# Kernel tuning notes

Hardware: AMD Instinct MI355X
Metric: run time of the kernel (lower is better)

The kernel has to match this reference:

```python
import jax, jax.numpy as jnp
import numpy as np

KERNEL_PARA = 1.0

def setup_inputs() -> dict:
    key = jax.random.key(0)
    k1, k2 = jax.random.split(key)
    H1 = jax.random.normal(k1, (8192, 64), dtype=jnp.float32)
    H2 = jax.random.normal(k2, (8192, 64), dtype=jnp.float32)
    return {"H1": H1, "H2": H2}

def reference(H1, H2):
    # S[ij] = exp(-delta * ||x_i - x_j||^2), via ||a||^2 + ||b||^2 - 2 a.b
    H11 = jnp.sum(H1 * H1, axis=1)[:, None]          # [n1, 1]
    H22 = jnp.sum(H2 * H2, axis=1)[None, :]          # [1, n2]
    H12 = jnp.matmul(H1, H2.T)                        # [n1, n2]
    D_2 = H11 + H22 - 2.0 * H12
    return jnp.exp(-KERNEL_PARA * D_2)
```

## Files before the change

### kernel.cpp

```cpp
#include <hip/hip_runtime.h>
#include <hip/hip_bf16.h>


typedef float  f32x4   __attribute__((ext_vector_type(4)));
typedef float  float4v __attribute__((ext_vector_type(4)));
typedef short  short8  __attribute__((ext_vector_type(8)));
typedef unsigned short ushort8 __attribute__((ext_vector_type(8)));

#define TM 128
#define TN 128
#define KD 64

__device__ __forceinline__ unsigned short f2bf(float x) {
    __hip_bfloat16 h = __float2bfloat16(x);
    unsigned short u;
    __builtin_memcpy(&u, &h, 2);
    return u;
}
__device__ __forceinline__ float bf2f(unsigned short u) {
    unsigned int v = ((unsigned int)u) << 16;
    float f;
    __builtin_memcpy(&f, &v, 4);
    return f;
}

__global__ __launch_bounds__(256, 2) void gauss_mfma(
    const float* __restrict__ H1, const float* __restrict__ H2,
    float* __restrict__ out, int N1, int N2)
{
    __shared__ __align__(16) unsigned short sAhi[TM * KD];
    __shared__ __align__(16) unsigned short sAlo[TM * KD];
    __shared__ __align__(16) unsigned short sBhi[TN * KD];
    __shared__ __align__(16) unsigned short sBlo[TN * KD];
    __shared__ float snrm[TM + TN];

    const int t = threadIdx.x;
    const int row0 = blockIdx.y * TM;
    const int col0 = blockIdx.x * TN;

    #pragma unroll
    for (int side = 0; side < 2; ++side) {
        const float* src = side ? (H2 + (size_t)col0 * KD)
                                : (H1 + (size_t)row0 * KD);
        unsigned short* hi = side ? sBhi : sAhi;
        unsigned short* lo = side ? sBlo : sAlo;
        #pragma unroll
        for (int i = 0; i < 4; ++i) {
            int g   = i * 256 + t;
            int row = g >> 3;
            int kc  = g & 7;
            const float4v* p = (const float4v*)(src + (size_t)g * 8);
            float4v v0 = p[0], v1 = p[1];
            ushort8 h, l;
            #pragma unroll
            for (int e = 0; e < 8; ++e) {
                float a = (e < 4) ? v0[e] : v1[e - 4];
                unsigned short hb = f2bf(a);
                float r = a - bf2f(hb);
                h[e] = hb;
                l[e] = f2bf(r);
            }
            unsigned int off = (unsigned)(row * (KD * 2) + kc * 16);
            off ^= (unsigned)((row & 7) << 4);
            *(ushort8*)((char*)hi + off) = h;
            *(ushort8*)((char*)lo + off) = l;
        }
    }
    __syncthreads();

    {
        const unsigned short* hi = (t < TM) ? sAhi : sBhi;
        const unsigned short* lo = (t < TM) ? sAlo : sBlo;
        int row = (t < TM) ? t : (t - TM);
        float s = 0.f;
        #pragma unroll
        for (int kc = 0; kc < 8; ++kc) {
            unsigned int off = (unsigned)(row * (KD * 2) + kc * 16)
                             ^ (unsigned)((row & 7) << 4);
            ushort8 h = *(const ushort8*)((const char*)hi + off);
            ushort8 l = *(const ushort8*)((const char*)lo + off);
            #pragma unroll
            for (int e = 0; e < 8; ++e) {
                float a = bf2f(h[e]) + bf2f(l[e]);
                s = fmaf(a, a, s);
            }
        }
        snrm[t] = s;
    }
    __syncthreads();

    const int lane = t & 63;
    const int w    = t >> 6;
    const int wr   = w >> 1, wc = w & 1;
    const int lr   = lane & 15;
    const int kb   = lane >> 4;

    f32x4 acc[4][4];
    #pragma unroll
    for (int a = 0; a < 4; ++a)
        #pragma unroll
        for (int b = 0; b < 4; ++b)
            acc[a][b] = (f32x4){0.f, 0.f, 0.f, 0.f};

    #pragma unroll
    for (int ks = 0; ks < 2; ++ks) {
        short8 bh[4], bl[4];
        #pragma unroll
        for (int fc = 0; fc < 4; ++fc) {
            int rowb = wc * 64 + fc * 16 + lr;
            unsigned int off = (unsigned)(rowb * (KD * 2) + ks * 64 + kb * 16)
                             ^ (unsigned)((rowb & 7) << 4);
            bh[fc] = *(const short8*)((const char*)sBhi + off);
            bl[fc] = *(const short8*)((const char*)sBlo + off);
        }
        #pragma unroll
        for (int fr = 0; fr < 4; ++fr) {
            int rowa = wr * 64 + fr * 16 + lr;
            unsigned int off = (unsigned)(rowa * (KD * 2) + ks * 64 + kb * 16)
                             ^ (unsigned)((rowa & 7) << 4);
            short8 ah = *(const short8*)((const char*)sAhi + off);
            short8 al = *(const short8*)((const char*)sAlo + off);
            #pragma unroll
            for (int fc = 0; fc < 4; ++fc) {
                acc[fr][fc] = __builtin_amdgcn_mfma_f32_16x16x32_bf16(
                                  ah, bh[fc], acc[fr][fc], 0, 0, 0);
                acc[fr][fc] = __builtin_amdgcn_mfma_f32_16x16x32_bf16(
                                  ah, bl[fc], acc[fr][fc], 0, 0, 0);
                acc[fr][fc] = __builtin_amdgcn_mfma_f32_16x16x32_bf16(
                                  al, bh[fc], acc[fr][fc], 0, 0, 0);
            }
        }
    }

    const int r4 = (lane >> 4) * 4;
    #pragma unroll
    for (int fr = 0; fr < 4; ++fr) {
        int rloc = wr * 64 + fr * 16 + r4;
        #pragma unroll
        for (int fc = 0; fc < 4; ++fc) {
            int cloc = wc * 64 + fc * 16 + lr;
            float n2v = snrm[TM + cloc];
            size_t gc = (size_t)(col0 + cloc);
            #pragma unroll
            for (int j = 0; j < 4; ++j) {
                float n1v = snrm[rloc + j];
                float d2  = n1v + n2v - 2.0f * acc[fr][fc][j];
                out[(size_t)(row0 + rloc + j) * (size_t)N2 + gc] = __expf(-d2);
            }
        }
    }
}

extern "C" void kernel_launch(void* const* d_in, const int* in_sizes, int n_in,
                              void* d_out, int out_size, void* d_ws, size_t ws_size,
                              hipStream_t stream) {
    const float* H1 = (const float*)d_in[0];
    const float* H2 = (const float*)d_in[1];
    float* out = (float*)d_out;
    const int n1 = in_sizes[0] / KD;
    const int n2 = in_sizes[1] / KD;
    dim3 grid(n2 / TN, n1 / TM);
    gauss_mfma<<<grid, dim3(256), 0, stream>>>(H1, H2, out, n1, n2);
}
```

Measured before the change: 56.59 us.

## Precompute bf16 hi/lo planes and norms in prep kernel, stage via direct LDS loads

Adds a prep kernel that splits H1/H2 into bf16 hi/lo panels already in the swizzled LDS layout and computes the row norms once into the workspace. The main kernel then copies those panels straight into LDS with global_load_lds, so each of the 4096 tiles no longer repeats the conversion and norm work. It also swaps the MFMA operand order so every lane ends up holding 4 contiguous output columns, which allows vectorized nontemporal stores. The cost is an extra launch plus workspace traffic, and the old path remains as a fallback when the workspace is too small.

```diff
diff --git a/kernel.cpp b/kernel.cpp
--- a/kernel.cpp
+++ b/kernel.cpp
@@ -2,14 +2,18 @@
 #include <hip/hip_bf16.h>
 
 
-typedef float  f32x4   __attribute__((ext_vector_type(4)));
-typedef float  float4v __attribute__((ext_vector_type(4)));
-typedef short  short8  __attribute__((ext_vector_type(8)));
+typedef float  f32x4  __attribute__((ext_vector_type(4)));
+typedef short  short8 __attribute__((ext_vector_type(8)));
 typedef unsigned short ushort8 __attribute__((ext_vector_type(8)));
 
+#define KD 64
 #define TM 128
 #define TN 128
-#define KD 64
+
+#define PLANE_BYTES (8192u * 64u * 2u)
+#define OFF_N1  (4u * PLANE_BYTES)
+#define OFF_N2  (4u * PLANE_BYTES + 8192u * 4u)
+#define WS_NEED ((size_t)(4u * PLANE_BYTES + 2u * 8192u * 4u))
 
 __device__ __forceinline__ unsigned short f2bf(float x) {
     __hip_bfloat16 h = __float2bfloat16(x);
@@ -24,76 +28,142 @@
     return f;
 }
 
-__global__ __launch_bounds__(256, 2) void gauss_mfma(
-    const float* __restrict__ H1, const float* __restrict__ H2,
-    float* __restrict__ out, int N1, int N2)
+__device__ __forceinline__ void gload_lds16(const void* g, void* l) {
+    __builtin_amdgcn_global_load_lds(
+        (const __attribute__((address_space(1))) unsigned char*)g,
+        (__attribute__((address_space(3))) unsigned char*)l, 16, 0, 0);
+}
+
+__device__ __forceinline__ unsigned panel_off(unsigned rin, unsigned kcByte) {
+    return (rin * 128u + kcByte) ^ ((rin & 7u) << 4);
+}
+
+__global__ __launch_bounds__(256) void gauss_prep(const float* __restrict__ H1,
+                                                  const float* __restrict__ H2,
+                                                  unsigned char* __restrict__ ws)
 {
-    __shared__ __align__(16) unsigned short sAhi[TM * KD];
-    __shared__ __align__(16) unsigned short sAlo[TM * KD];
-    __shared__ __align__(16) unsigned short sBhi[TN * KD];
-    __shared__ __align__(16) unsigned short sBlo[TN * KD];
-    __shared__ float snrm[TM + TN];
-
-    const int t = threadIdx.x;
+    const int cid   = blockIdx.x * 256 + threadIdx.x;
+    const int which = cid >> 16;
+    const int g     = cid & 65535;
+    const int row   = g >> 3;
+    const int kc    = g & 7;
+
+    const float* src = which ? H2 : H1;
+    const f32x4* p = (const f32x4*)(src + (size_t)g * 8);
+    f32x4 v0 = p[0], v1 = p[1];
+
+    ushort8 h, l;
+    float s = 0.f;
+    #pragma unroll
+    for (int e = 0; e < 8; ++e) {
+        float a = (e < 4) ? v0[e] : v1[e - 4];
+        unsigned short hb = f2bf(a);
+        h[e] = hb;
+        l[e] = f2bf(a - bf2f(hb));
+        s = fmaf(a, a, s);
+    }
+    s += __shfl_xor(s, 1);
+    s += __shfl_xor(s, 2);
+    s += __shfl_xor(s, 4);
+
+    const unsigned rin = (unsigned)(row & 127);
+    const size_t  pb   = (size_t)(row >> 7) * 16384u + panel_off(rin, (unsigned)kc * 16u);
+    unsigned char* hi = ws + (which ? 2u * PLANE_BYTES : 0u) + pb;
+    unsigned char* lo = ws + (which ? 3u * PLANE_BYTES : PLANE_BYTES) + pb;
+    *(ushort8*)hi = h;
+    *(ushort8*)lo = l;
+    if (kc == 0)
+        *(float*)(ws + (which ? OFF_N2 : OFF_N1) + (size_t)row * 4u) = s;
+}
+
+template <bool STAGED>
+__global__ __launch_bounds__(256, 2) void gauss_main(const float* __restrict__ H1,
+                                                     const float* __restrict__ H2,
+                                                     const unsigned char* __restrict__ ws,
+                                                     float* __restrict__ out, int n2dim)
+{
+    __shared__ __align__(16) unsigned char smem[65536];
+    __shared__ __align__(16) float snrm[TM + TN];
+
+    const int t    = threadIdx.x;
+    const int lane = t & 63, w = t >> 6;
+    const int wr = w >> 1, wc = w & 1;
+    const int lr = lane & 15, kb = lane >> 4;
+    const int r4 = kb * 4;
     const int row0 = blockIdx.y * TM;
     const int col0 = blockIdx.x * TN;
 
-    #pragma unroll
-    for (int side = 0; side < 2; ++side) {
-        const float* src = side ? (H2 + (size_t)col0 * KD)
-                                : (H1 + (size_t)row0 * KD);
-        unsigned short* hi = side ? sBhi : sAhi;
-        unsigned short* lo = side ? sBlo : sAlo;
-        #pragma unroll
-        for (int i = 0; i < 4; ++i) {
-            int g   = i * 256 + t;
-            int row = g >> 3;
-            int kc  = g & 7;
-            const float4v* p = (const float4v*)(src + (size_t)g * 8);
-            float4v v0 = p[0], v1 = p[1];
-            ushort8 h, l;
+    float n1v[4];
+    f32x4 n2v[4];
+
+    if (STAGED) {
+        const float* nrm1 = (const float*)(ws + OFF_N1);
+        const float* nrm2 = (const float*)(ws + OFF_N2);
+        #pragma unroll
+        for (int fr = 0; fr < 4; ++fr)
+            n1v[fr] = nrm1[row0 + wr * 64 + fr * 16 + lr];
+        #pragma unroll
+        for (int fc = 0; fc < 4; ++fc)
+            n2v[fc] = *(const f32x4*)(nrm2 + col0 + wc * 64 + fc * 16 + r4);
+
+        const size_t pa = (size_t)(row0 >> 7) * 16384u;
+        const size_t pb = (size_t)(col0 >> 7) * 16384u;
+        #pragma unroll
+        for (int it = 0; it < 16; ++it) {
+            const int region = it >> 2;
+            const size_t panel = (region < 2) ? pa : pb;
+            const unsigned char* gsrc = ws + (size_t)region * PLANE_BYTES + panel
+                                      + (size_t)(it & 3) * 4096u + (size_t)t * 16u;
+            gload_lds16(gsrc, smem + it * 4096 + w * 1024);
+        }
+    } else {
+        #pragma unroll
+        for (int side = 0; side < 2; ++side) {
+            const float* src = side ? (H2 + (size_t)col0 * KD) : (H1 + (size_t)row0 * KD);
+            unsigned char* hi = (unsigned char*)smem + (side ? 32768 : 0);
+            unsigned char* lo = hi + 16384;
             #pragma unroll
-            for (int e = 0; e < 8; ++e) {
-                float a = (e < 4) ? v0[e] : v1[e - 4];
-                unsigned short hb = f2bf(a);
-                float r = a - bf2f(hb);
-                h[e] = hb;
-                l[e] = f2bf(r);
+            for (int i = 0; i < 4; ++i) {
+                int g   = i * 256 + t;
+                int row = g >> 3;
+                int kc  = g & 7;
+                const f32x4* p = (const f32x4*)(src + (size_t)g * 8);
+                f32x4 v0 = p[0], v1 = p[1];
+                ushort8 h, l;
+                float s = 0.f;
+                #pragma unroll
+                for (int e = 0; e < 8; ++e) {
+                    float a = (e < 4) ? v0[e] : v1[e - 4];
+                    unsigned short hb = f2bf(a);
+                    h[e] = hb;
+                    l[e] = f2bf(a - bf2f(hb));
+                    s = fmaf(a, a, s);
+                }
+                s += __shfl_xor(s, 1);
+                s += __shfl_xor(s, 2);
+                s += __shfl_xor(s, 4);
+                unsigned off = panel_off((unsigned)row, (unsigned)kc * 16u);
+                *(ushort8*)(hi + off) = h;
+                *(ushort8*)(lo + off) = l;
+                if (kc == 0) snrm[side * TM + row] = s;
             }
-            unsigned int off = (unsigned)(row * (KD * 2) + kc * 16);
-            off ^= (unsigned)((row & 7) << 4);
-            *(ushort8*)((char*)hi + off) = h;
-            *(ushort8*)((char*)lo + off) = l;
         }
     }
     __syncthreads();
 
-    {
-        const unsigned short* hi = (t < TM) ? sAhi : sBhi;
-        const unsigned short* lo = (t < TM) ? sAlo : sBlo;
-        int row = (t < TM) ? t : (t - TM);
-        float s = 0.f;
-        #pragma unroll
-        for (int kc = 0; kc < 8; ++kc) {
-            unsigned int off = (unsigned)(row * (KD * 2) + kc * 16)
-                             ^ (unsigned)((row & 7) << 4);
-            ushort8 h = *(const ushort8*)((const char*)hi + off);
-            ushort8 l = *(const ushort8*)((const char*)lo + off);
-            #pragma unroll
-            for (int e = 0; e < 8; ++e) {
-                float a = bf2f(h[e]) + bf2f(l[e]);
-                s = fmaf(a, a, s);
-            }
-        }
-        snrm[t] = s;
-    }
-    __syncthreads();
-
-    const int lane = t & 63;
-    const int w    = t >> 6;
-    const int wr   = w >> 1, wc = w & 1;
-    const int lr   = lane & 15;
-    const int kb   = lane >> 4;
+    if (!STAGED) {
+        #pragma unroll
+        for (int fr = 0; fr < 4; ++fr)
+            n1v[fr] = snrm[wr * 64 + fr * 16 + lr];
+        #pragma unroll
+        for (int fc = 0; fc < 4; ++fc)
+            n2v[fc] = *(const f32x4*)&snrm[TM + wc * 64 + fc * 16 + r4];
+    }
+
+    const unsigned char* sAhi = smem;
+    const unsigned char* sAlo = smem + 16384;
+    const unsigned char* sBhi = smem + 32768;
+    const unsigned char* sBlo = smem + 49152;
 
     f32x4 acc[4][4];
     #pragma unroll
@@ -104,49 +174,43 @@
 
     #pragma unroll
     for (int ks = 0; ks < 2; ++ks) {
-        short8 bh[4], bl[4];
+        const unsigned kByte = (unsigned)(ks * 64 + kb * 16);
+        short8 ah[4], al[4];
+        #pragma unroll
+        for (int fr = 0; fr < 4; ++fr) {
+            const unsigned rowa = (unsigned)(wr * 64 + fr * 16 + lr);
+            const unsigned off  = panel_off(rowa, kByte);
+            ah[fr] = *(const short8*)(sAhi + off);
+            al[fr] = *(const short8*)(sAlo + off);
+        }
         #pragma unroll
         for (int fc = 0; fc < 4; ++fc) {
-            int rowb = wc * 64 + fc * 16 + lr;
-            unsigned int off = (unsigned)(rowb * (KD * 2) + ks * 64 + kb * 16)
-                             ^ (unsigned)((rowb & 7) << 4);
-            bh[fc] = *(const short8*)((const char*)sBhi + off);
-            bl[fc] = *(const short8*)((const char*)sBlo + off);
-        }
-        #pragma unroll
-        for (int fr = 0; fr < 4; ++fr) {
-            int rowa = wr * 64 + fr * 16 + lr;
-            unsigned int off = (unsigned)(rowa * (KD * 2) + ks * 64 + kb * 16)
-                             ^ (unsigned)((rowa & 7) << 4);
-            short8 ah = *(const short8*)((const char*)sAhi + off);
-            short8 al = *(const short8*)((const char*)sAlo + off);
+            const unsigned rowb = (unsigned)(wc * 64 + fc * 16 + lr);
+            const unsigned off  = panel_off(rowb, kByte);
+            short8 bh = *(const short8*)(sBhi + off);
+            short8 bl = *(const short8*)(sBlo + off);
             #pragma unroll
-            for (int fc = 0; fc < 4; ++fc) {
-                acc[fr][fc] = __builtin_amdgcn_mfma_f32_16x16x32_bf16(
-                                  ah, bh[fc], acc[fr][fc], 0, 0, 0);
-                acc[fr][fc] = __builtin_amdgcn_mfma_f32_16x16x32_bf16(
-                                  ah, bl[fc], acc[fr][fc], 0, 0, 0);
-                acc[fr][fc] = __builtin_amdgcn_mfma_f32_16x16x32_bf16(
-                                  al, bh[fc], acc[fr][fc], 0, 0, 0);
+            for (int fr = 0; fr < 4; ++fr) {
+                acc[fr][fc] = __builtin_amdgcn_mfma_f32_16x16x32_bf16(bh, ah[fr], acc[fr][fc], 0, 0, 0);
+                acc[fr][fc] = __builtin_amdgcn_mfma_f32_16x16x32_bf16(bl, ah[fr], acc[fr][fc], 0, 0, 0);
+                acc[fr][fc] = __builtin_amdgcn_mfma_f32_16x16x32_bf16(bh, al[fr], acc[fr][fc], 0, 0, 0);
             }
         }
     }
 
-    const int r4 = (lane >> 4) * 4;
     #pragma unroll
     for (int fr = 0; fr < 4; ++fr) {
-        int rloc = wr * 64 + fr * 16 + r4;
+        const int grow = row0 + wr * 64 + fr * 16 + lr;
+        float* orow = out + (size_t)grow * (size_t)n2dim + (col0 + wc * 64 + r4);
         #pragma unroll
         for (int fc = 0; fc < 4; ++fc) {
-            int cloc = wc * 64 + fc * 16 + lr;
-            float n2v = snrm[TM + cloc];
-            size_t gc = (size_t)(col0 + cloc);
+            f32x4 cst;
             #pragma unroll
             for (int j = 0; j < 4; ++j) {
-                float n1v = snrm[rloc + j];
-                float d2  = n1v + n2v - 2.0f * acc[fr][fc][j];
-                out[(size_t)(row0 + rloc + j) * (size_t)N2 + gc] = __expf(-d2);
+                float d2 = fmaf(-2.0f, acc[fr][fc][j], n1v[fr] + n2v[fc][j]);
+                cst[j] = __expf(-d2);
             }
+            __builtin_nontemporal_store(cst, (f32x4*)(orow + fc * 16));
         }
     }
 }
@@ -160,5 +224,11 @@
     const int n1 = in_sizes[0] / KD;
     const int n2 = in_sizes[1] / KD;
     dim3 grid(n2 / TN, n1 / TM);
-    gauss_mfma<<<grid, dim3(256), 0, stream>>>(H1, H2, out, n1, n2);
-}
+
+    if (ws_size >= WS_NEED) {
+        gauss_prep<<<dim3(512), dim3(256), 0, stream>>>(H1, H2, (unsigned char*)d_ws);
+        gauss_main<true><<<grid, dim3(256), 0, stream>>>(H1, H2, (const unsigned char*)d_ws, out, n2);
+    } else {
+        gauss_main<false><<<grid, dim3(256), 0, stream>>>(H1, H2, nullptr, out, n2);
+    }
+}
```

After: 78.85 us. 39.3% more time.
